# Kernel optimization log

Hardware: AMD Instinct MI355X
Metric: run time of the kernel (lower is better)

## Reference

```python
import jax, jax.numpy as jnp
import numpy as np

NUM_LAYERS, NUM_HEADS, DH, C = 5, 4, 32, 128
B, T, HH, WW = 2, 12, 32, 32


def conv2d(x, w, b):
    # x: (N, Cin, H, W), w: (Cout, Cin, 3, 3) same padding
    y = jax.lax.conv_general_dilated(x, w, window_strides=(1, 1), padding='SAME',
                                     dimension_numbers=('NCHW', 'OIHW', 'NCHW'))
    return y + b[None, :, None, None]


def sine_pos(length, depth):
    pos = jnp.arange(length, dtype=jnp.float32)[:, None]
    div = jnp.exp(jnp.arange(0, depth, 2, dtype=jnp.float32) * (-np.log(10000.0) / depth))
    pe = jnp.zeros((length, depth), dtype=jnp.float32)
    pe = pe.at[:, 0::2].set(jnp.sin(pos * div))
    pe = pe.at[:, 1::2].set(jnp.cos(pos * div))
    return pe[None, :, :, None, None]  # (1, L, dh, 1, 1) broadcasts over batch & spatial


def group_norm(x, scale, bias, groups=4, eps=1e-5):
    n, c, h, w = x.shape
    xg = x.reshape(n, groups, c // groups, h, w)
    mu = xg.mean(axis=(2, 3, 4), keepdims=True)
    var = ((xg - mu) ** 2).mean(axis=(2, 3, 4), keepdims=True)
    xg = (xg - mu) * jax.lax.rsqrt(var + eps)
    return xg.reshape(n, c, h, w) * scale[None, :, None, None] + bias[None, :, None, None]


def head_forward(x, pos, qw, qb, kvw, kvb, aw, ab):
    # x: (B, L, dh, H, W)
    b, l, c, h, w = x.shape
    xf = x.reshape(b * l, c, h, w)
    q = conv2d(xf, qw, qb).reshape(b, l, c, h, w) + pos
    v = conv2d(xf, kvw, kvb).reshape(b, l, c, h, w)  # k and v share features
    k = v + pos
    # pairwise concat: (B, Lq, Lk, 2*dh, H, W)
    qe = jnp.broadcast_to(q[:, :, None], (b, l, l, c, h, w))
    ke = jnp.broadcast_to(k[:, None, :], (b, l, l, c, h, w))
    qk = jnp.concatenate([qe, ke], axis=3).reshape(b * l * l, 2 * c, h, w)
    att = conv2d(qk, aw, ab).reshape(b, l, l, 1, h, w)
    att = jax.nn.softmax(att, axis=2)  # softmax over key-frame axis
    return jnp.sum(att * v[:, None], axis=2)  # (B, L, dh, H, W)


def reference(input_tensor, q_w, q_b, kv_w, kv_b, att_w, att_b,
              ff1_w, ff1_b, ff2_w, ff2_b, gn_w, gn_b):
    num_layers, num_heads = q_w.shape[0], q_w.shape[1]
    b, l, c, h, w = input_tensor.shape
    dh = c // num_heads
    pos = sine_pos(l, dh)
    out = input_tensor
    for li in range(num_layers):
        heads = [head_forward(out[:, :, i * dh:(i + 1) * dh], pos,
                              q_w[li, i], q_b[li, i], kv_w[li, i], kv_b[li, i],
                              att_w[li, i], att_b[li, i])
                 for i in range(num_heads)]
        att_out = jnp.concatenate(heads, axis=2) + out  # residual
        att_flat = att_out.reshape(b * l, c, h, w)
        ff = conv2d(jax.nn.relu(conv2d(att_flat, ff1_w[li], ff1_b[li])), ff2_w[li], ff2_b[li])
        y = group_norm(ff + att_flat, gn_w[li], gn_b[li])
        out = y.reshape(b, l, c, h, w)
    return out


def setup_inputs() -> dict:
    key = jax.random.key(0)
    ks = jax.random.split(key, 12)
    f = lambda k, s, sc=1.0: jax.random.normal(k, s, dtype=jnp.float32) * sc
    L, H = NUM_LAYERS, NUM_HEADS
    return {
        'input_tensor': f(ks[0], (B, T, C, HH, WW)),
        'q_w': f(ks[1], (L, H, DH, DH, 3, 3), 0.05),
        'q_b': f(ks[2], (L, H, DH), 0.05),
        'kv_w': f(ks[3], (L, H, DH, DH, 3, 3), 0.05),
        'kv_b': f(ks[4], (L, H, DH), 0.05),
        'att_w': f(ks[5], (L, H, 1, 2 * DH, 3, 3), 0.05),
        'att_b': f(ks[6], (L, H, 1), 0.05),
        'ff1_w': f(ks[7], (L, C, C, 3, 3), 0.03),
        'ff1_b': f(ks[8], (L, C), 0.03),
        'ff2_w': f(ks[9], (L, C, C, 3, 3), 0.03),
        'ff2_b': f(ks[10], (L, C), 0.03),
        'gn_w': jnp.ones((L, C), dtype=jnp.float32),
        'gn_b': jnp.zeros((L, C), dtype=jnp.float32),
    }
```

## Files before the change

kernel.cpp:

```cpp
#include <hip/hip_runtime.h>

#define NELEM 3145728
#define IMG 24
#define CH 128
#define HW 1024

using short8   = __attribute__((ext_vector_type(8))) short;
using ushort4v = __attribute__((ext_vector_type(4))) unsigned short;
using float4v  = __attribute__((ext_vector_type(4))) float;
using float16v = __attribute__((ext_vector_type(16))) float;

__device__ inline unsigned short f2bf(float f){
    union { float f; unsigned u; } c; c.f = f;
    return (unsigned short)((c.u + 0x7FFF + ((c.u >> 16) & 1)) >> 16);
}

__global__ __launch_bounds__(256) void k_prep(
    const float* __restrict__ ff1w, const float* __restrict__ ff2w,
    const float* __restrict__ kvw, const float* __restrict__ input,
    unsigned short* __restrict__ Wd, unsigned short* __restrict__ Wkv,
    float* __restrict__ cur)
{
    const int t = threadIdx.x;
    __shared__ float tile[32 * 132];
    if (blockIdx.x < 5760) {
        int idx = blockIdx.x * 256 + t;
        int li2 = idx / 147456, r1 = idx - li2 * 147456;
        int j = r1 & 7, co = (r1 >> 3) & 127;
        int kh = (r1 >> 10) & 1, k16 = (r1 >> 11) & 7, tap = r1 >> 14;
        int ci = k16 * 16 + kh * 8 + j;
        const float* base = ((li2 & 1) ? ff2w : ff1w) + (size_t)(li2 >> 1) * 147456;
        Wd[idx] = f2bf(base[(co * 128 + ci) * 9 + tap]);
    } else if (blockIdx.x < 6480) {
        int idx = (blockIdx.x - 5760) * 256 + t;
        int li = idx / 36864, r1 = idx - li * 36864;
        int j = r1 & 7, co = (r1 >> 3) & 127;
        int kh = (r1 >> 10) & 1, k16 = (r1 >> 11) & 1, tap = r1 >> 12;
        int h = co >> 5, colc = co & 31, cil = k16 * 16 + kh * 8 + j;
        Wkv[idx] = f2bf(kvw[((size_t)((li * 4 + h) * 32 + colc) * 32 + cil) * 9 + tap]);
    } else {
        int bb = blockIdx.x - 6480;
        int img = bb >> 5, px0 = (bb & 31) * 32;
        #pragma unroll
        for (int it = 0; it < 4; it++) {
            int c = it * 32 + (t >> 3), pxq = t & 7;
            float4v val = *(const float4v*)(input + ((size_t)img * 128 + c) * HW + px0 + pxq * 4);
            #pragma unroll
            for (int j = 0; j < 4; j++) tile[(pxq * 4 + j) * 132 + c] = val[j];
        }
        __syncthreads();
        #pragma unroll
        for (int it = 0; it < 4; it++) {
            int px = it * 8 + (t >> 5), cq = t & 31;
            float4v o = *(float4v*)(tile + px * 132 + cq * 4);
            *(float4v*)(cur + ((size_t)img * HW + px0 + px) * 128 + cq * 4) = o;
        }
    }
}

__global__ __launch_bounds__(256, 2) void k_kvattn(
    const float* __restrict__ cur, const unsigned short* __restrict__ wkv,
    const float* __restrict__ kvb, const float* __restrict__ aw,
    const float* __restrict__ pstatp, const float* __restrict__ gw,
    const float* __restrict__ gb, float* __restrict__ v,
    float* __restrict__ ak, float* __restrict__ pstatz)
{
    const int img = blockIdx.x, h = blockIdx.y, y0 = blockIdx.z * 8;
    const int t = threadIdx.x;
    const int b = img / 12, l = img - b * 12;

    if (blockIdx.x == 0 && blockIdx.y == 0 && blockIdx.z == 0 && t < 192)
        pstatz[t] = 0.f;

    __shared__ float sxv[32 * 341];
    __shared__ unsigned short slab[408 * 40];
    __shared__ float spos[32], sbias[32], sgw[32], sgb[32];

    if (t < 32) {
        int j2 = t & ~1;
        float freq = __expf(-(float)j2 * 0.28782313662425576f);
        float ang = (float)l * freq;
        spos[t] = (t & 1) ? __cosf(ang) : __sinf(ang);
        sbias[t] = kvb[h * 32 + t];
        sgw[t] = gw ? gw[h * 32 + t] : 1.f;
        sgb[t] = gb ? gb[h * 32 + t] : 0.f;
    }
    float mu = 0.f, inv = 1.f;
    if (pstatp) {
        float S = pstatp[(img * 4 + h) * 2], Q = pstatp[(img * 4 + h) * 2 + 1];
        mu = S * (1.f / 32768.f);
        inv = rsqrtf(Q * (1.f / 32768.f) - mu * mu + 1e-5f);
    }
    __syncthreads();

    for (int u = t; u < 3264; u += 256) {
        int q = u & 7, p = u >> 3;
        int lr = p / 34, lc = p - lr * 34;
        int yr = y0 - 2 + lr, x = lc - 1;
        float4v val = (float4v){0.f, 0.f, 0.f, 0.f};
        if (yr >= 0 && yr < 32 && x >= 0 && x < 32) {
            val = *(const float4v*)(cur + ((size_t)img * HW + yr * 32 + x) * 128 + h * 32 + q * 4);
            #pragma unroll
            for (int j = 0; j < 4; j++)
                val[j] = (val[j] - mu) * inv * sgw[q * 4 + j] + sgb[q * 4 + j];
        }
        ushort4v o;
        #pragma unroll
        for (int j = 0; j < 4; j++) o[j] = f2bf(val[j]);
        *(ushort4v*)(slab + p * 40 + q * 4) = o;
    }
    __syncthreads();

    const int lane = t & 63, wave = t >> 6;
    const int colx = lane & 31, kh = lane >> 5;
    const short8* w8 = reinterpret_cast<const short8*>(wkv);

    for (int f = wave; f < 10; f += 4) {
        float16v acc;
        #pragma unroll
        for (int r = 0; r < 16; r++) acc[r] = 0.f;
        #pragma unroll
        for (int tap = 0; tap < 9; tap++) {
            const int ky = tap / 3, kx = tap - ky * 3;
            #pragma unroll
            for (int k16 = 0; k16 < 2; k16++) {
                short8 a = *reinterpret_cast<const short8*>(
                    slab + ((f + ky) * 34 + colx + kx) * 40 + k16 * 16 + kh * 8);
                short8 bf = w8[((tap * 2 + k16) * 2 + kh) * 128 + h * 32 + colx];
                acc = __builtin_amdgcn_mfma_f32_32x32x16_bf16(a, bf, acc, 0, 0, 0);
            }
        }
        const int yr = y0 - 1 + f;
        const bool rowin = (yr >= 0 && yr < 32);
        const bool vown = rowin && f >= 1 && f <= 8;
        const float posci = spos[colx], bb = sbias[colx];
        float* vrow = v + ((size_t)img * HW + yr * 32) * 128 + h * 32 + colx;
        #pragma unroll
        for (int r = 0; r < 16; r++) {
            int x2 = (r & 3) + 8 * (r >> 2) + 4 * kh;
            float val = rowin ? acc[r] + bb : 0.f;
            if (vown) vrow[(size_t)x2 * 128] = val;
            sxv[colx * 341 + f * 34 + x2 + 1] = rowin ? val + posci : 0.f;
        }
    }
    for (int u = t; u < 640; u += 256) {
        int ci = u & 31, r2 = u >> 5;
        sxv[ci * 341 + (r2 >> 1) * 34 + ((r2 & 1) ? 33 : 0)] = 0.f;
    }
    __syncthreads();

    const float* wb = aw + (h * 64 + 32) * 9;
    const int r = t >> 5, xx = t & 31;
    float acc2 = 0.f;
    #pragma unroll 4
    for (int ci = 0; ci < 32; ci++) {
        #pragma unroll
        for (int ky = 0; ky < 3; ky++)
            #pragma unroll
            for (int kx = 0; kx < 3; kx++)
                acc2 = fmaf(sxv[ci * 341 + (r + ky) * 34 + xx + kx],
                            wb[ci * 9 + ky * 3 + kx], acc2);
    }
    ak[((size_t)(b * 4 + h) * 12 + l) * HW + (y0 + r) * 32 + xx] = acc2;
}

__global__ __launch_bounds__(256, 2) void k_ffn(
    const float* __restrict__ cin, const unsigned short* __restrict__ w1,
    const float* __restrict__ b1, const unsigned short* __restrict__ w2,
    const float* __restrict__ b2, float* __restrict__ cout,
    float* __restrict__ pstat)
{
    const int img = blockIdx.x, y = blockIdx.y;
    const int t = threadIdx.x;
    const int wave = t >> 6, lane = t & 63;
    const int colx = lane & 31, kh = lane >> 5;
    const int cog = wave * 32;

    __shared__ __align__(16) char smem[46240];
    unsigned short* s1 = (unsigned short*)smem;
    unsigned short* s2 = (unsigned short*)smem;

    for (int u = t; u < 5440; u += 256) {
        int q = u & 31, p = u >> 5;
        int lr = p / 34, lc = p - lr * 34;
        int yr = y - 2 + lr, x = lc - 1;
        float4v val = (float4v){0.f, 0.f, 0.f, 0.f};
        if (yr >= 0 && yr < 32 && x >= 0 && x < 32)
            val = *(const float4v*)(cin + ((size_t)img * HW + yr * 32 + x) * 128 + q * 4);
        ushort4v o;
        #pragma unroll
        for (int j = 0; j < 4; j++) o[j] = f2bf(val[j]);
        *(ushort4v*)(s1 + p * 136 + q * 4) = o;
    }

    const short8* w8a = reinterpret_cast<const short8*>(w1);
    const short8* w8b = reinterpret_cast<const short8*>(w2);
    const int bl = kh * 128 + cog + colx;

    float16v acc[3];
    #pragma unroll
    for (int f = 0; f < 3; f++)
        #pragma unroll
        for (int r = 0; r < 16; r++) acc[f][r] = 0.f;

    short8 B9[2][9];
    #pragma unroll
    for (int tap = 0; tap < 9; tap++)
        B9[0][tap] = w8a[(tap * 8 + 0) * 256 + bl];

    __syncthreads();

    #pragma unroll
    for (int k16 = 0; k16 < 8; k16++) {
        if (k16 + 1 < 8) {
            #pragma unroll
            for (int tap = 0; tap < 9; tap++)
                B9[(k16 + 1) & 1][tap] = w8a[(tap * 8 + k16 + 1) * 256 + bl];
        }
        #pragma unroll
        for (int ar = 0; ar < 5; ar++) {
            #pragma unroll
            for (int kx = 0; kx < 3; kx++) {
                short8 a = *reinterpret_cast<const short8*>(
                    s1 + (ar * 34 + kx + colx) * 136 + kh * 8 + k16 * 16);
                #pragma unroll
                for (int ky = 0; ky < 3; ky++) {
                    const int f = ar - ky;
                    if (f >= 0 && f < 3)
                        acc[f] = __builtin_amdgcn_mfma_f32_32x32x16_bf16(
                            a, B9[k16 & 1][ky * 3 + kx], acc[f], 0, 0, 0);
                }
            }
        }
    }

    short8 bfr[2][8];
    auto loadB2 = [&](int tap, int buf){
        #pragma unroll
        for (int k16 = 0; k16 < 8; k16++)
            bfr[buf][k16] = w8b[(tap * 8 + k16) * 256 + bl];
    };
    loadB2(0, 0);
    __syncthreads();

    {
        const int co = cog + colx;
        const float bb1 = b1[co];
        #pragma unroll
        for (int f = 0; f < 3; f++) {
            const bool rowin = (y - 1 + f >= 0) && (y - 1 + f < 32);
            #pragma unroll
            for (int r = 0; r < 16; r++) {
                int x2 = (r & 3) + 8 * (r >> 2) + 4 * kh;
                float val = rowin ? fmaxf(acc[f][r] + bb1, 0.f) : 0.f;
                s2[(f * 34 + x2 + 1) * 136 + co] = f2bf(val);
            }
        }
    }
    for (int u = t; u < 768; u += 256) {
        int c = u & 127, rr = u >> 7;
        s2[((rr >> 1) * 34 + ((rr & 1) ? 33 : 0)) * 136 + c] = 0;
    }
    __syncthreads();

    const int co = cog + colx;
    float res[16];
    #pragma unroll
    for (int r = 0; r < 16; r++) {
        int x2 = (r & 3) + 8 * (r >> 2) + 4 * kh;
        res[r] = cin[((size_t)img * HW + y * 32 + x2) * 128 + co];
    }

    float16v a2;
    #pragma unroll
    for (int r = 0; r < 16; r++) a2[r] = 0.f;
    #pragma unroll
    for (int tap = 0; tap < 9; tap++) {
        if (tap + 1 < 9) loadB2(tap + 1, (tap + 1) & 1);
        const int ky = tap / 3, kx = tap - ky * 3;
        #pragma unroll
        for (int k16 = 0; k16 < 8; k16++) {
            short8 a = *reinterpret_cast<const short8*>(
                s2 + (ky * 34 + kx + colx) * 136 + kh * 8 + k16 * 16);
            a2 = __builtin_amdgcn_mfma_f32_32x32x16_bf16(a, bfr[tap & 1][k16], a2, 0, 0, 0);
        }
    }

    const float bb2 = b2[co];
    float ps1 = 0.f, ps2 = 0.f;
    #pragma unroll
    for (int r = 0; r < 16; r++) {
        int x2 = (r & 3) + 8 * (r >> 2) + 4 * kh;
        float val = a2[r] + bb2 + res[r];
        cout[((size_t)img * HW + y * 32 + x2) * 128 + co] = val;
        ps1 += val; ps2 += val * val;
    }
    #pragma unroll
    for (int o = 32; o > 0; o >>= 1) {
        ps1 += __shfl_xor(ps1, o); ps2 += __shfl_xor(ps2, o);
    }
    if (lane == 0) {
        atomicAdd(&pstat[(img * 4 + wave) * 2], ps1);
        atomicAdd(&pstat[(img * 4 + wave) * 2 + 1], ps2);
    }
}

__global__ __launch_bounds__(256) void k_wsum(const float* __restrict__ ak,
    const float* __restrict__ v, float* __restrict__ cur,
    const float* __restrict__ pstatp, const float* __restrict__ gw,
    const float* __restrict__ gb)
{
    int gid = blockIdx.x * 256 + threadIdx.x;
    int c = gid & 127, px = (gid >> 7) & 1023, b = gid >> 17;
    int h = c >> 5;
    const float* wp = ak + ((size_t)(b * 4 + h) * 12) * HW + px;
    float a[12], m = -1e30f;
    #pragma unroll
    for (int l = 0; l < 12; l++) { a[l] = wp[l * HW]; m = fmaxf(m, a[l]); }
    float ssum = 0.f;
    #pragma unroll
    for (int l = 0; l < 12; l++) { a[l] = __expf(a[l] - m); ssum += a[l]; }
    float invs = 1.f / ssum;
    const float* vp = v + ((size_t)(b * 12) * HW + px) * 128 + c;
    float s = 0.f;
    #pragma unroll
    for (int l = 0; l < 12; l++) s += a[l] * vp[(size_t)l * HW * 128];
    s *= invs;
    float gwv = gw ? gw[c] : 1.f, gbv = gb ? gb[c] : 0.f;
    float* cp = cur + ((size_t)(b * 12) * HW + px) * 128 + c;
    #pragma unroll
    for (int l = 0; l < 12; l++) {
        int img = b * 12 + l;
        float mu = 0.f, inv = 1.f;
        if (pstatp) {
            float S = pstatp[(img * 4 + h) * 2], Q = pstatp[(img * 4 + h) * 2 + 1];
            mu = S * (1.f / 32768.f);
            inv = rsqrtf(Q * (1.f / 32768.f) - mu * mu + 1e-5f);
        }
        float cv = cp[(size_t)l * HW * 128];
        cp[(size_t)l * HW * 128] = (cv - mu) * inv * gwv + gbv + s;
    }
}

__global__ __launch_bounds__(256) void k_gnlast(const float* __restrict__ y,
    const float* __restrict__ pstat, const float* __restrict__ gw,
    const float* __restrict__ gb, float* __restrict__ outp)
{
    int gid = blockIdx.x * 256 + threadIdx.x;
    int px4 = (gid & 255) * 4, c = (gid >> 8) & 127, img = gid >> 15;
    int g = c >> 5;
    float S = pstat[(img * 4 + g) * 2], Q = pstat[(img * 4 + g) * 2 + 1];
    float mu = S * (1.f / 32768.f);
    float inv = rsqrtf(Q * (1.f / 32768.f) - mu * mu + 1e-5f);
    float gg = gw[c], bb = gb[c];
    float4v o;
    #pragma unroll
    for (int j = 0; j < 4; j++) {
        float val = y[((size_t)img * HW + px4 + j) * 128 + c];
        o[j] = (val - mu) * inv * gg + bb;
    }
    *(float4v*)(outp + ((size_t)img * 128 + c) * HW + px4) = o;
}

extern "C" void kernel_launch(void* const* d_in, const int* in_sizes, int n_in,
                              void* d_out, int out_size, void* d_ws, size_t ws_size,
                              hipStream_t stream)
{
    const float* input = (const float*)d_in[0];
    const float* kv_w  = (const float*)d_in[3];
    const float* kv_b  = (const float*)d_in[4];
    const float* att_w = (const float*)d_in[5];
    const float* ff1_w = (const float*)d_in[7];
    const float* ff1_b = (const float*)d_in[8];
    const float* ff2_w = (const float*)d_in[9];
    const float* ff2_b = (const float*)d_in[10];
    const float* gn_w  = (const float*)d_in[11];
    const float* gn_b  = (const float*)d_in[12];

    float* ws  = (float*)d_ws;
    float* c0  = ws;
    float* c1  = c0 + (size_t)NELEM;
    float* ak  = c1 + (size_t)NELEM;
    float* pstat = ak + 98304;
    unsigned short* W2d  = (unsigned short*)(pstat + 384);
    unsigned short* W2kv = W2d + 1474560;
    float* v    = (float*)d_out;
    float* outp = (float*)d_out;

    k_prep<<<7248, 256, 0, stream>>>(ff1_w, ff2_w, kv_w, input, W2d, W2kv, c0);

    for (int li = 0; li < 5; li++) {
        float* cin  = (li & 1) ? c1 : c0;
        float* cout = (li & 1) ? c0 : c1;
        float* psC = pstat + (li & 1) * 192;
        const float* psP = li ? pstat + ((li - 1) & 1) * 192 : nullptr;
        const float* gwP = li ? gn_w + (li - 1) * 128 : nullptr;
        const float* gbP = li ? gn_b + (li - 1) * 128 : nullptr;

        k_kvattn<<<dim3(IMG, 4, 4), 256, 0, stream>>>(
            cin, W2kv + (size_t)li * 36864, kv_b + li * 128, att_w + (size_t)li * 2304,
            psP, gwP, gbP, v, ak, psC);
        k_wsum<<<1024, 256, 0, stream>>>(ak, v, cin, psP, gwP, gbP);
        k_ffn<<<dim3(IMG, 32), 256, 0, stream>>>(
            cin, W2d + (size_t)(li * 2 + 0) * 147456, ff1_b + li * 128,
            W2d + (size_t)(li * 2 + 1) * 147456, ff2_b + li * 128, cout, psC);
    }
    k_gnlast<<<3072, 256, 0, stream>>>(c1, pstat + 0, gn_w + 4 * 128,
                                       gn_b + 4 * 128, outp);
}
```

Baseline: 440.0 us.

## Split FFN input staging into channel halves and drop weight double-buffering for occupancy

The first conv's input tile is now staged in LDS in two 64-channel halves instead of all 128 channels at once, shrinking shared memory from about 46KB to about 27KB. The double-buffered weight registers in both conv stages are replaced by single buffers, and launch bounds go from 2 to 5 blocks per CU, so more waves can be resident. The cost is an extra staging pass and barrier. Weight loads are no longer prefetched ahead of the MFMAs, so load latency is exposed unless the added occupancy hides it.

```diff
diff --git a/kernel.cpp b/kernel.cpp
--- a/kernel.cpp
+++ b/kernel.cpp
@@ -164,7 +164,7 @@
     ak[((size_t)(b * 4 + h) * 12 + l) * HW + (y0 + r) * 32 + xx] = acc2;
 }
 
-__global__ __launch_bounds__(256, 2) void k_ffn(
+__global__ __launch_bounds__(256, 5) void k_ffn(
     const float* __restrict__ cin, const unsigned short* __restrict__ w1,
     const float* __restrict__ b1, const unsigned short* __restrict__ w2,
     const float* __restrict__ b2, float* __restrict__ cout,
@@ -176,22 +176,9 @@
     const int colx = lane & 31, kh = lane >> 5;
     const int cog = wave * 32;
 
-    __shared__ __align__(16) char smem[46240];
-    unsigned short* s1 = (unsigned short*)smem;
-    unsigned short* s2 = (unsigned short*)smem;
-
-    for (int u = t; u < 5440; u += 256) {
-        int q = u & 31, p = u >> 5;
-        int lr = p / 34, lc = p - lr * 34;
-        int yr = y - 2 + lr, x = lc - 1;
-        float4v val = (float4v){0.f, 0.f, 0.f, 0.f};
-        if (yr >= 0 && yr < 32 && x >= 0 && x < 32)
-            val = *(const float4v*)(cin + ((size_t)img * HW + yr * 32 + x) * 128 + q * 4);
-        ushort4v o;
-        #pragma unroll
-        for (int j = 0; j < 4; j++) o[j] = f2bf(val[j]);
-        *(ushort4v*)(s1 + p * 136 + q * 4) = o;
-    }
+    __shared__ __align__(16) char smem[27744];
+    unsigned short* s1h = (unsigned short*)smem;
+    unsigned short* s2  = (unsigned short*)smem;
 
     const short8* w8a = reinterpret_cast<const short8*>(w1);
     const short8* w8b = reinterpret_cast<const short8*>(w2);
@@ -203,45 +190,56 @@
         #pragma unroll
         for (int r = 0; r < 16; r++) acc[f][r] = 0.f;
 
-    short8 B9[2][9];
-    #pragma unroll
-    for (int tap = 0; tap < 9; tap++)
-        B9[0][tap] = w8a[(tap * 8 + 0) * 256 + bl];
-
-    __syncthreads();
-
-    #pragma unroll
-    for (int k16 = 0; k16 < 8; k16++) {
-        if (k16 + 1 < 8) {
+    #pragma unroll
+    for (int half = 0; half < 2; half++) {
+        for (int u = t; u < 2720; u += 256) {
+            int q = u & 15, p = u >> 4;
+            int lr = p / 34, lc = p - lr * 34;
+            int yr = y - 2 + lr, x = lc - 1;
+            float4v val = (float4v){0.f, 0.f, 0.f, 0.f};
+            if (yr >= 0 && yr < 32 && x >= 0 && x < 32)
+                val = *(const float4v*)(cin + ((size_t)img * HW + yr * 32 + x) * 128
+                                        + half * 64 + q * 4);
+            ushort4v o;
+            #pragma unroll
+            for (int j = 0; j < 4; j++) o[j] = f2bf(val[j]);
+            *(ushort4v*)(s1h + p * 72 + q * 4) = o;
+        }
+        __syncthreads();
+
+        #pragma unroll
+        for (int k16l = 0; k16l < 4; k16l++) {
+            const int k16 = half * 4 + k16l;
+            short8 B9[9];
             #pragma unroll
             for (int tap = 0; tap < 9; tap++)
-                B9[(k16 + 1) & 1][tap] = w8a[(tap * 8 + k16 + 1) * 256 + bl];
-        }
-        #pragma unroll
-        for (int ar = 0; ar < 5; ar++) {
-            #pragma unroll
-            for (int kx = 0; kx < 3; kx++) {
-                short8 a = *reinterpret_cast<const short8*>(
-                    s1 + (ar * 34 + kx + colx) * 136 + kh * 8 + k16 * 16);
+                B9[tap] = w8a[(tap * 8 + k16) * 256 + bl];
+            #pragma unroll
+            for (int ar = 0; ar < 5; ar++) {
                 #pragma unroll
-                for (int ky = 0; ky < 3; ky++) {
-                    const int f = ar - ky;
-                    if (f >= 0 && f < 3)
-                        acc[f] = __builtin_amdgcn_mfma_f32_32x32x16_bf16(
-                            a, B9[k16 & 1][ky * 3 + kx], acc[f], 0, 0, 0);
+                for (int kx = 0; kx < 3; kx++) {
+                    short8 a = *reinterpret_cast<const short8*>(
+                        s1h + (ar * 34 + kx + colx) * 72 + kh * 8 + k16l * 16);
+                    #pragma unroll
+                    for (int ky = 0; ky < 3; ky++) {
+                        const int f = ar - ky;
+                        if (f >= 0 && f < 3)
+                            acc[f] = __builtin_amdgcn_mfma_f32_32x32x16_bf16(
+                                a, B9[ky * 3 + kx], acc[f], 0, 0, 0);
+                    }
                 }
             }
         }
-    }
-
-    short8 bfr[2][8];
-    auto loadB2 = [&](int tap, int buf){
+        __syncthreads();
+    }
+
+    short8 bfr[8];
+    auto loadB2 = [&](int tap){
         #pragma unroll
         for (int k16 = 0; k16 < 8; k16++)
-            bfr[buf][k16] = w8b[(tap * 8 + k16) * 256 + bl];
+            bfr[k16] = w8b[(tap * 8 + k16) * 256 + bl];
     };
-    loadB2(0, 0);
-    __syncthreads();
+    loadB2(0);
 
     {
         const int co = cog + colx;
@@ -276,13 +274,13 @@
     for (int r = 0; r < 16; r++) a2[r] = 0.f;
     #pragma unroll
     for (int tap = 0; tap < 9; tap++) {
-        if (tap + 1 < 9) loadB2(tap + 1, (tap + 1) & 1);
+        if (tap) loadB2(tap);
         const int ky = tap / 3, kx = tap - ky * 3;
         #pragma unroll
         for (int k16 = 0; k16 < 8; k16++) {
             short8 a = *reinterpret_cast<const short8*>(
                 s2 + (ky * 34 + kx + colx) * 136 + kh * 8 + k16 * 16);
-            a2 = __builtin_amdgcn_mfma_f32_32x32x16_bf16(a, bfr[tap & 1][k16], a2, 0, 0, 0);
+            a2 = __builtin_amdgcn_mfma_f32_32x32x16_bf16(a, bfr[k16], a2, 0, 0, 0);
         }
     }
 
```

Result: slower. 560.3 us (+27.3%).

## Register-block the attention conv epilogue and split channels across waves

Applied to the files above, without the earlier changes.

Rewrites the 3x3 single-output attention conv in k_kvattn so each thread computes four adjacent x outputs from a shared row of six loaded values, with the 32 input channels split across the four waves. The partial sums are then reduced through shared memory, reusing the slab buffer, and stored as float4. The shared feature tile's row stride changes to 35 and its channel stride to 353, likely to change LDS bank mapping. The aim is fewer LDS loads per FMA, in exchange for an extra barrier and a reduction done by only one wave.

```diff
diff --git a/kernel.cpp b/kernel.cpp
--- a/kernel.cpp
+++ b/kernel.cpp
@@ -72,8 +72,8 @@
     if (blockIdx.x == 0 && blockIdx.y == 0 && blockIdx.z == 0 && t < 192)
         pstatz[t] = 0.f;
 
-    __shared__ float sxv[32 * 341];
-    __shared__ unsigned short slab[408 * 40];
+    __shared__ float sxv[32 * 353];
+    __shared__ __align__(16) unsigned short slab[408 * 40];
     __shared__ float spos[32], sbias[32], sgw[32], sgb[32];
 
     if (t < 32) {
@@ -140,28 +140,48 @@
             int x2 = (r & 3) + 8 * (r >> 2) + 4 * kh;
             float val = rowin ? acc[r] + bb : 0.f;
             if (vown) vrow[(size_t)x2 * 128] = val;
-            sxv[colx * 341 + f * 34 + x2 + 1] = rowin ? val + posci : 0.f;
+            sxv[colx * 353 + f * 35 + x2 + 1] = rowin ? val + posci : 0.f;
         }
     }
     for (int u = t; u < 640; u += 256) {
         int ci = u & 31, r2 = u >> 5;
-        sxv[ci * 341 + (r2 >> 1) * 34 + ((r2 & 1) ? 33 : 0)] = 0.f;
-    }
-    __syncthreads();
-
-    const float* wb = aw + (h * 64 + 32) * 9;
-    const int r = t >> 5, xx = t & 31;
-    float acc2 = 0.f;
-    #pragma unroll 4
-    for (int ci = 0; ci < 32; ci++) {
-        #pragma unroll
-        for (int ky = 0; ky < 3; ky++)
-            #pragma unroll
-            for (int kx = 0; kx < 3; kx++)
-                acc2 = fmaf(sxv[ci * 341 + (r + ky) * 34 + xx + kx],
-                            wb[ci * 9 + ky * 3 + kx], acc2);
-    }
-    ak[((size_t)(b * 4 + h) * 12 + l) * HW + (y0 + r) * 32 + xx] = acc2;
+        sxv[ci * 353 + (r2 >> 1) * 35 + ((r2 & 1) ? 33 : 0)] = 0.f;
+    }
+    __syncthreads();
+
+    const int g = wave, u2 = lane;
+    const int rr = u2 >> 3, x0 = (u2 & 7) * 4;
+    const float* wbg = aw + (h * 64 + 32) * 9 + g * 72;
+    float4v pacc = (float4v){0.f, 0.f, 0.f, 0.f};
+    #pragma unroll
+    for (int ci = 0; ci < 8; ci++) {
+        const float* sp = sxv + (g * 8 + ci) * 353 + rr * 35 + x0;
+        const float* wp = wbg + ci * 9;
+        #pragma unroll
+        for (int ky = 0; ky < 3; ky++) {
+            float f0 = sp[ky*35+0], f1 = sp[ky*35+1], f2 = sp[ky*35+2];
+            float f3 = sp[ky*35+3], f4 = sp[ky*35+4], f5 = sp[ky*35+5];
+            float w0 = wp[ky*3+0], w1 = wp[ky*3+1], w2f = wp[ky*3+2];
+            pacc[0] = fmaf(f2, w2f, fmaf(f1, w1, fmaf(f0, w0, pacc[0])));
+            pacc[1] = fmaf(f3, w2f, fmaf(f2, w1, fmaf(f1, w0, pacc[1])));
+            pacc[2] = fmaf(f4, w2f, fmaf(f3, w1, fmaf(f2, w0, pacc[2])));
+            pacc[3] = fmaf(f5, w2f, fmaf(f4, w1, fmaf(f3, w0, pacc[3])));
+        }
+    }
+    float4v* sred = reinterpret_cast<float4v*>(slab);
+    sred[g * 64 + u2] = pacc;
+    __syncthreads();
+    if (t < 64) {
+        float4v s = sred[t];
+        #pragma unroll
+        for (int gg = 1; gg < 4; gg++) {
+            float4v o = sred[gg * 64 + t];
+            #pragma unroll
+            for (int j = 0; j < 4; j++) s[j] += o[j];
+        }
+        *reinterpret_cast<float4v*>(ak + ((size_t)(b * 4 + h) * 12 + l) * HW
+                                    + (y0 + (t >> 3)) * 32 + (t & 7) * 4) = s;
+    }
 }
 
 __global__ __launch_bounds__(256, 2) void k_ffn(
```

After: 432.4 us. Within noise of the previous version (-1.7%).
